# Optimization experiments

Measured on AMD Instinct MI355X. Metric: run time of the kernel, lower is better.

## Reference

```python
import jax, jax.numpy as jnp
import numpy as np

D = 1024
H = 16
HD = D // H
FF = 4 * D


def layer_norm(x, gamma, beta, eps=1e-5):
    mu = jnp.mean(x, axis=-1, keepdims=True)
    var = jnp.var(x, axis=-1, keepdims=True)
    return (x - mu) * jax.lax.rsqrt(var + eps) * gamma + beta


def setup_inputs() -> dict:
    key = jax.random.key(0)
    ks = jax.random.split(key, 12)
    B, Nq, Nkv = 8, 512, 1024
    s = 0.02
    return {
        "query": jax.random.normal(ks[0], (B, Nq, D), jnp.float32),
        "key_value": jax.random.normal(ks[1], (B, Nkv, D), jnp.float32),
        "key_padding_mask": jax.random.randint(ks[2], (B, Nkv), 0, 2) > 0,
        "nq_gamma": jnp.ones((D,), jnp.float32),
        "nq_beta": jnp.zeros((D,), jnp.float32),
        "nkv_gamma": jnp.ones((D,), jnp.float32),
        "nkv_beta": jnp.zeros((D,), jnp.float32),
        "in_proj_w": jax.random.normal(ks[3], (3 * D, D), jnp.float32) * s,
        "in_proj_b": jnp.zeros((3 * D,), jnp.float32),
        "out_w": jax.random.normal(ks[4], (D, D), jnp.float32) * s,
        "out_b": jnp.zeros((D,), jnp.float32),
        "nff_gamma": jnp.ones((D,), jnp.float32),
        "nff_beta": jnp.zeros((D,), jnp.float32),
        "ff1_w": jax.random.normal(ks[5], (FF, D), jnp.float32) * s,
        "ff1_b": jnp.zeros((FF,), jnp.float32),
        "ff2_w": jax.random.normal(ks[6], (D, FF), jnp.float32) * s,
        "ff2_b": jnp.zeros((D,), jnp.float32),
    }


def reference(query, key_value, key_padding_mask, nq_gamma, nq_beta, nkv_gamma,
              nkv_beta, in_proj_w, in_proj_b, out_w, out_b, nff_gamma, nff_beta,
              ff1_w, ff1_b, ff2_w, ff2_b):
    B, Nq, _ = query.shape
    Nkv = key_value.shape[1]

    q_in = layer_norm(query, nq_gamma, nq_beta)
    kv_in = layer_norm(key_value, nkv_gamma, nkv_beta)

    # packed in-projection as in torch MultiheadAttention
    wq, wk, wv = in_proj_w[:D], in_proj_w[D:2 * D], in_proj_w[2 * D:]
    bq, bk, bv = in_proj_b[:D], in_proj_b[D:2 * D], in_proj_b[2 * D:]
    q = (q_in @ wq.T + bq).reshape(B, Nq, H, HD).transpose(0, 2, 1, 3)   # b h q d
    k = (kv_in @ wk.T + bk).reshape(B, Nkv, H, HD).transpose(0, 2, 1, 3)  # b h k d
    v = (kv_in @ wv.T + bv).reshape(B, Nkv, H, HD).transpose(0, 2, 1, 3)

    scale = 1.0 / np.sqrt(HD).astype(np.float32)
    scores = jnp.einsum('bhqd,bhkd->bhqk', q, k) * scale
    neg = jnp.finfo(scores.dtype).min
    scores = jnp.where(key_padding_mask[:, None, None, :], neg, scores)
    attn = jax.nn.softmax(scores, axis=-1)                  # (B,H,Nq,Nkv)
    ctx = jnp.einsum('bhqk,bhkd->bhqd', attn, v)
    ctx = ctx.transpose(0, 2, 1, 3).reshape(B, Nq, D)
    attended = ctx @ out_w.T + out_b
    attn_weights = jnp.mean(attn, axis=1)                   # averaged over heads

    x = query + attended
    h = layer_norm(x, nff_gamma, nff_beta)
    h = jax.nn.gelu(h @ ff1_w.T + ff1_b, approximate=False)
    x = x + (h @ ff2_w.T + ff2_b)
    return (x, attn_weights)
```

## Files before the change

### kernel.cpp

```cpp
#include <hip/hip_runtime.h>
#include <hip/hip_bf16.h>
#include <math.h>

#define D    1024
#define NQ   512
#define NKV  1024
#define BATCH 8
#define NH   16
#define HD   64
#define FFD  4096

typedef short bf16x8 __attribute__((ext_vector_type(8)));
typedef float f32x4  __attribute__((ext_vector_type(4)));

static __device__ __forceinline__ float bf2f(__hip_bfloat16 x){ return __bfloat162float(x); }
static __device__ __forceinline__ unsigned short f2bbits(float f){
    __hip_bfloat16 h = __float2bfloat16(f);
    return *(unsigned short*)&h;
}

static __device__ __forceinline__ void gload_lds16(const __hip_bfloat16* g, __hip_bfloat16* l){
    __builtin_amdgcn_global_load_lds(
        (const __attribute__((address_space(1))) void*)g,
        (__attribute__((address_space(3))) void*)l,
        16, 0, 0);
}

__global__ __launch_bounds__(256) void cvt_w_kernel(const float* __restrict__ in,
                                                    __hip_bfloat16* __restrict__ out, int n)
{
    int i = blockIdx.x*256 + threadIdx.x;
    if (i < n) out[i] = __float2bfloat16(in[i]);
}

__global__ __launch_bounds__(256) void ln_kernel(
    const float* __restrict__ x, const float* __restrict__ gamma, const float* __restrict__ beta,
    __hip_bfloat16* __restrict__ out)
{
    int row = blockIdx.x, t = threadIdx.x;
    __shared__ float wsum[4];
    __shared__ float stat[2];
    float4 v = *(const float4*)&x[(size_t)row*D + t*4];
    float s = v.x+v.y+v.z+v.w;
    #pragma unroll
    for (int o=32;o>0;o>>=1) s += __shfl_down(s, o);
    if ((t&63)==0) wsum[t>>6] = s;
    __syncthreads();
    if (t==0) stat[0] = (wsum[0]+wsum[1]+wsum[2]+wsum[3])*(1.f/D);
    __syncthreads();
    float mu = stat[0];
    float d0=v.x-mu, d1=v.y-mu, d2=v.z-mu, d3=v.w-mu;
    float s2 = d0*d0+d1*d1+d2*d2+d3*d3;
    #pragma unroll
    for (int o=32;o>0;o>>=1) s2 += __shfl_down(s2, o);
    if ((t&63)==0) wsum[t>>6] = s2;
    __syncthreads();
    if (t==0) stat[1] = rsqrtf((wsum[0]+wsum[1]+wsum[2]+wsum[3])*(1.f/D) + 1e-5f);
    __syncthreads();
    float rs = stat[1];
    const float4 g = *(const float4*)&gamma[t*4];
    const float4 b = *(const float4*)&beta[t*4];
    union { unsigned short u[4]; short4 s4; } pk;
    pk.u[0]=f2bbits(d0*rs*g.x+b.x); pk.u[1]=f2bbits(d1*rs*g.y+b.y);
    pk.u[2]=f2bbits(d2*rs*g.z+b.z); pk.u[3]=f2bbits(d3*rs*g.w+b.w);
    *(short4*)&out[(size_t)row*D + t*4] = pk.s4;
}

#define BM 128
#define BN 128
#define BK 32
__global__ __launch_bounds__(256) void gemm_mfma_kernel(
    const __hip_bfloat16* __restrict__ A, const __hip_bfloat16* __restrict__ Wb,
    const float* __restrict__ bias, int biasOff,
    const float* __restrict__ residIn, const float* __restrict__ residF,
    float* __restrict__ Cf, __hip_bfloat16* __restrict__ Cb,
    int M, int N, int K, int gelu, int vtrans)
{
    __shared__ __hip_bfloat16 As[BM*BK];
    __shared__ __hip_bfloat16 Bs[BN*BK];
    int t = threadIdx.x;
    int w = t >> 6, lane = t & 63;
    int quad = lane >> 4, l16 = lane & 15;
    int bm = blockIdx.y * BM, bn = blockIdx.x * BN;
    int wm = (w >> 1) * 64, wn = (w & 1) * 64;
    const int srow = lane >> 2, scol = (lane & 3) << 3;
    f32x4 acc[4][4];
    #pragma unroll
    for (int i=0;i<4;i++)
        #pragma unroll
        for (int j=0;j<4;j++) acc[i][j] = (f32x4){0.f,0.f,0.f,0.f};

    for (int k0 = 0; k0 < K; k0 += BK){
        #pragma unroll
        for (int rep = 0; rep < 2; rep++){
            int ti = (w << 1) + rep;
            gload_lds16(&A [(size_t)(bm + ti*16 + srow)*K + k0 + scol], &As[ti*16*BK]);
            gload_lds16(&Wb[(size_t)(bn + ti*16 + srow)*K + k0 + scol], &Bs[ti*16*BK]);
        }
        __syncthreads();
        bf16x8 af[4], bfr[4];
        #pragma unroll
        for (int i=0;i<4;i++) af[i]  = *(const bf16x8*)&As[(wm + 16*i + l16)*BK + quad*8];
        #pragma unroll
        for (int j=0;j<4;j++) bfr[j] = *(const bf16x8*)&Bs[(wn + 16*j + l16)*BK + quad*8];
        #pragma unroll
        for (int i=0;i<4;i++)
            #pragma unroll
            for (int j=0;j<4;j++)
                acc[i][j] = __builtin_amdgcn_mfma_f32_16x16x32_bf16(af[i], bfr[j], acc[i][j], 0, 0, 0);
        __syncthreads();
    }
    #pragma unroll
    for (int i=0;i<4;i++){
        #pragma unroll
        for (int j=0;j<4;j++){
            int colg = bn + wn + 16*j + l16;
            if (vtrans){
                union { unsigned short u[4]; short4 s4; } pk;
                #pragma unroll
                for (int r=0;r<4;r++){
                    float vv = acc[i][j][r] + bias[biasOff + colg];
                    pk.u[r] = f2bbits(vv);
                }
                int rowg0 = bm + wm + 16*i + quad*4;
                int bb = rowg0 >> 10, kv = rowg0 & 1023;
                int hh = colg >> 6,  dd = colg & 63;
                *(short4*)&Cb[(((size_t)bb*NH + hh)*HD + dd)*NKV + kv] = pk.s4;
            } else {
                #pragma unroll
                for (int r=0;r<4;r++){
                    int rowg = bm + wm + 16*i + quad*4 + r;
                    float vv = acc[i][j][r] + bias[biasOff + colg];
                    if (gelu) vv = 0.5f*vv*(1.f + erff(vv*0.70710678118654752f));
                    size_t idx = (size_t)rowg*N + colg;
                    if (residIn) vv += residIn[idx];
                    if (residF)  vv += residF[idx];
                    if (Cf) Cf[idx] = vv;
                    if (Cb) Cb[idx] = __float2bfloat16(vv);
                }
            }
        }
    }
}

#define QT 16
#define PLD (NKV + 8)
__global__ __launch_bounds__(512) void attn_kernel(
    const __hip_bfloat16* __restrict__ q, const __hip_bfloat16* __restrict__ k,
    const __hip_bfloat16* __restrict__ vt, const void* __restrict__ mask,
    __hip_bfloat16* __restrict__ ctx, float* __restrict__ attn_out)
{
    const int t = threadIdx.x;
    const int w = t >> 6;
    const int lane = t & 63;
    const int g = lane >> 4;
    const int l16 = lane & 15;
    const int b  = blockIdx.x;
    const int q0 = blockIdx.y * QT;

    __shared__ __hip_bfloat16 P[QT*PLD];
    __shared__ float pvred[4*16*20];
    __shared__ float red[8*16];
    __shared__ int m8s;

    if (t==0) m8s = 0;
    __syncthreads();
    if (t < 256){ unsigned wd = ((const unsigned*)mask)[t]; if (wd > 1u) atomicOr(&m8s, 1); }
    __syncthreads();
    const bool m8 = m8s != 0;

    unsigned mbits = 0;
    #pragma unroll
    for (int kt=0;kt<8;kt++){
        #pragma unroll
        for (int r=0;r<4;r++){
            size_t mi = (size_t)b*NKV + w*128 + kt*16 + 4*g + r;
            int mv = m8 ? (int)((const unsigned char*)mask)[mi] : ((const int*)mask)[mi];
            if (mv) mbits |= (1u << (kt*4+r));
        }
    }

    float amean[8][4];
    #pragma unroll
    for (int kt=0;kt<8;kt++)
        #pragma unroll
        for (int r=0;r<4;r++) amean[kt][r] = 0.f;

    const int mt = w >> 1;
    const int kvh = w & 1;
    const __hip_bfloat16* qrow = &q[((size_t)(b*NQ + q0 + l16))*D];

    for (int h=0; h<NH; h++){
        bf16x8 bq0 = *(const bf16x8*)&qrow[h*HD + g*8];
        bf16x8 bq1 = *(const bf16x8*)&qrow[h*HD + 32 + g*8];
        f32x4 s[8];
        #pragma unroll
        for (int kt=0;kt<8;kt++){
            const __hip_bfloat16* kp = &k[((size_t)(b*NKV + w*128 + kt*16 + l16))*D + h*HD];
            bf16x8 a0 = *(const bf16x8*)&kp[g*8];
            bf16x8 a1 = *(const bf16x8*)&kp[32 + g*8];
            f32x4 z = (f32x4){0.f,0.f,0.f,0.f};
            z = __builtin_amdgcn_mfma_f32_16x16x32_bf16(a0, bq0, z, 0, 0, 0);
            z = __builtin_amdgcn_mfma_f32_16x16x32_bf16(a1, bq1, z, 0, 0, 0);
            s[kt] = z;
        }
        float lmax = -3.0e38f;
        #pragma unroll
        for (int kt=0;kt<8;kt++){
            #pragma unroll
            for (int r=0;r<4;r++){
                float sv = ((mbits >> (kt*4+r)) & 1u) ? -3.0e38f : s[kt][r]*0.125f;
                s[kt][r] = sv;
                lmax = fmaxf(lmax, sv);
            }
        }
        lmax = fmaxf(lmax, __shfl_xor(lmax, 16));
        lmax = fmaxf(lmax, __shfl_xor(lmax, 32));
        if (lane < 16) red[w*16 + l16] = lmax;
        __syncthreads();
        float m = red[l16];
        #pragma unroll
        for (int w2=1; w2<8; w2++) m = fmaxf(m, red[w2*16 + l16]);
        float lsum = 0.f;
        #pragma unroll
        for (int kt=0;kt<8;kt++){
            #pragma unroll
            for (int r=0;r<4;r++){
                float e = __expf(s[kt][r] - m);
                s[kt][r] = e;
                lsum += e;
            }
        }
        lsum += __shfl_xor(lsum, 16);
        lsum += __shfl_xor(lsum, 32);
        __syncthreads();
        if (lane < 16) red[w*16 + l16] = lsum;
        __syncthreads();
        float tot = red[l16];
        #pragma unroll
        for (int w2=1; w2<8; w2++) tot += red[w2*16 + l16];
        float inv = 1.f/tot;
        float ai  = inv * (1.f/NH);
        #pragma unroll
        for (int kt=0;kt<8;kt++){
            union { unsigned short u[4]; short4 s4; } pk;
            #pragma unroll
            for (int r=0;r<4;r++){
                amean[kt][r] += s[kt][r]*ai;
                pk.u[r] = f2bbits(s[kt][r]);
            }
            *(short4*)&P[l16*PLD + w*128 + kt*16 + 4*g] = pk.s4;
        }
        __syncthreads();
        f32x4 pv = (f32x4){0.f,0.f,0.f,0.f};
        const __hip_bfloat16* vrow = &vt[(((size_t)(b*NH + h))*HD + mt*16 + l16)*NKV + kvh*512];
        #pragma unroll
        for (int ks=0;ks<16;ks++){
            bf16x8 av = *(const bf16x8*)&vrow[ks*32 + g*8];
            bf16x8 bp = *(const bf16x8*)&P[l16*PLD + kvh*512 + ks*32 + g*8];
            pv = __builtin_amdgcn_mfma_f32_16x16x32_bf16(av, bp, pv, 0, 0, 0);
        }
        if (kvh){
            *(f32x4*)&pvred[(mt*16 + l16)*20 + 4*g] = pv;
        }
        __syncthreads();
        if (!kvh){
            const f32x4 other = *(const f32x4*)&pvred[(mt*16 + l16)*20 + 4*g];
            union { unsigned short u[4]; short4 s4; } pk;
            #pragma unroll
            for (int r=0;r<4;r++) pk.u[r] = f2bbits((pv[r] + other[r]) * inv);
            *(short4*)&ctx[((size_t)(b*NQ + q0 + l16))*D + h*HD + mt*16 + 4*g] = pk.s4;
        }
        __syncthreads();
    }
    float* ao = attn_out + ((size_t)(b*NQ + q0 + l16))*NKV;
    #pragma unroll
    for (int kt=0;kt<8;kt++){
        float4 v4 = make_float4(amean[kt][0], amean[kt][1], amean[kt][2], amean[kt][3]);
        *(float4*)&ao[w*128 + kt*16 + 4*g] = v4;
    }
}

__global__ __launch_bounds__(256) void fill_f32_kernel(float* __restrict__ p, float val, long n){
    size_t i = (size_t)blockIdx.x*256 + threadIdx.x;
    if ((long)i < n) p[i] = val;
}

extern "C" void kernel_launch(void* const* d_in, const int* in_sizes, int n_in,
                              void* d_out, int out_size, void* d_ws, size_t ws_size,
                              hipStream_t stream)
{
    const float* query     = (const float*)d_in[0];
    const float* key_value = (const float*)d_in[1];
    const void*  mask      = d_in[2];
    const float* nq_gamma  = (const float*)d_in[3];
    const float* nq_beta   = (const float*)d_in[4];
    const float* nkv_gamma = (const float*)d_in[5];
    const float* nkv_beta  = (const float*)d_in[6];
    const float* ipw       = (const float*)d_in[7];
    const float* ipb       = (const float*)d_in[8];
    const float* out_w     = (const float*)d_in[9];
    const float* out_b     = (const float*)d_in[10];
    const float* nffg      = (const float*)d_in[11];
    const float* nffb      = (const float*)d_in[12];
    const float* ff1w      = (const float*)d_in[13];
    const float* ff1b      = (const float*)d_in[14];
    const float* ff2w      = (const float*)d_in[15];
    const float* ff2b      = (const float*)d_in[16];

    float* out_x = (float*)d_out;
    long Dn  = (n_in > 3)  ? in_sizes[3]  : 0;
    long FFn = (n_in > 14) ? in_sizes[14] : 0;
    long Rq=0, Rkv=0, Nkvd=0, Bd=0, Nqd=0;
    auto derive = [&](long Sq_, long Skv_)->bool{
        if (Dn <= 0 || Sq_ <= 0 || Skv_ <= 0) return false;
        if (Sq_ % Dn || Skv_ % Dn) return false;
        Rq = Sq_/Dn; Rkv = Skv_/Dn;
        long num = (long)out_size - Rq*Dn;
        if (Rq <= 0 || num <= 0 || num % Rq) return false;
        Nkvd = num / Rq;
        if (Nkvd <= 0 || Rkv % Nkvd) return false;
        Bd = Rkv / Nkvd;
        if (Bd <= 0 || Rq % Bd) return false;
        Nqd = Rq / Bd;
        if ((long)in_sizes[2] != Rkv) return false;
        return true;
    };
    int sentinel = 0;
    if (n_in != 17) sentinel = 600;
    else if (!derive(in_sizes[0], in_sizes[1])) sentinel = 300;
    if (!sentinel && !(Dn==1024 && FFn==4096 && Bd==8 && Nqd==512 && Nkvd==1024)) sentinel = 500;
    if (!sentinel && ws_size < ((size_t)88<<20)) sentinel = 400;
    if (sentinel){
        long n = out_size;
        fill_f32_kernel<<<(unsigned)((n+255)/256), 256, 0, stream>>>(out_x, (float)sentinel, n);
        return;
    }

    float* out_attn = out_x + (size_t)BATCH*NQ*D;

    char* Wc = (char*)d_ws;
    __hip_bfloat16* wip  = (__hip_bfloat16*)(Wc);
    __hip_bfloat16* wout = (__hip_bfloat16*)(Wc + ((size_t)6<<20));
    __hip_bfloat16* wff1 = (__hip_bfloat16*)(Wc + ((size_t)8<<20));
    __hip_bfloat16* wff2 = (__hip_bfloat16*)(Wc + ((size_t)16<<20));
    __hip_bfloat16* qln  = (__hip_bfloat16*)(Wc + ((size_t)24<<20));
    __hip_bfloat16* kvln = (__hip_bfloat16*)(Wc + ((size_t)32<<20));
    __hip_bfloat16* qb   = (__hip_bfloat16*)(Wc + ((size_t)48<<20));
    __hip_bfloat16* kb   = (__hip_bfloat16*)(Wc + ((size_t)56<<20));
    __hip_bfloat16* vbT  = (__hip_bfloat16*)(Wc + ((size_t)72<<20));
    __hip_bfloat16* ctx  = (__hip_bfloat16*)(Wc + ((size_t)24<<20));
    float*          x1   = (float*)(Wc + ((size_t)32<<20));
    __hip_bfloat16* hln  = (__hip_bfloat16*)(Wc + ((size_t)48<<20));
    __hip_bfloat16* hge  = (__hip_bfloat16*)(Wc + ((size_t)56<<20));

    cvt_w_kernel<<<(3*1024*1024+255)/256, 256, 0, stream>>>(ipw,  wip,  3*1024*1024);
    cvt_w_kernel<<<(1024*1024+255)/256,   256, 0, stream>>>(out_w, wout, 1024*1024);
    cvt_w_kernel<<<(4*1024*1024+255)/256, 256, 0, stream>>>(ff1w, wff1, 4*1024*1024);
    cvt_w_kernel<<<(4*1024*1024+255)/256, 256, 0, stream>>>(ff2w, wff2, 4*1024*1024);
    ln_kernel<<<BATCH*NQ,  256, 0, stream>>>(query,     nq_gamma,  nq_beta,  qln);
    ln_kernel<<<BATCH*NKV, 256, 0, stream>>>(key_value, nkv_gamma, nkv_beta, kvln);
    gemm_mfma_kernel<<<dim3(8,32),  256, 0, stream>>>(qln,  wip,                 ipb, 0,   nullptr, nullptr, nullptr, qb,  4096, 1024, 1024, 0, 0);
    gemm_mfma_kernel<<<dim3(8,64),  256, 0, stream>>>(kvln, wip + (size_t)D*D,   ipb, D,   nullptr, nullptr, nullptr, kb,  8192, 1024, 1024, 0, 0);
    gemm_mfma_kernel<<<dim3(8,64),  256, 0, stream>>>(kvln, wip + (size_t)2*D*D, ipb, 2*D, nullptr, nullptr, nullptr, vbT, 8192, 1024, 1024, 0, 1);
    attn_kernel<<<dim3(BATCH, NQ/QT), 512, 0, stream>>>(qb, kb, vbT, mask, ctx, out_attn);
    gemm_mfma_kernel<<<dim3(8,32),  256, 0, stream>>>(ctx, wout, out_b, 0, query, nullptr, x1, nullptr, 4096, 1024, 1024, 0, 0);
    ln_kernel<<<4096, 256, 0, stream>>>(x1, nffg, nffb, hln);
    gemm_mfma_kernel<<<dim3(32,32), 256, 0, stream>>>(hln, wff1, ff1b, 0, nullptr, nullptr, nullptr, hge, 4096, 4096, 1024, 1, 0);
    gemm_mfma_kernel<<<dim3(8,32),  256, 0, stream>>>(hge, wff2, ff2b, 0, nullptr, x1, out_x, nullptr, 4096, 1024, 4096, 0, 0);
}
```

Before: 690.9 us.

## Double-buffer GEMM LDS staging and merge Q/K/V projections into one launch

The GEMM main loop now uses two LDS buffers, so the async global-to-LDS load of the next K tile is issued before the MFMA work on the current tile, overlapping memory with compute and halving barriers per tile. The three separate Q, K and V projection launches are replaced by one qkv_kernel with a flat grid. In that grid the K and V projections share one GEMM over the packed weight rows (N=2048), and the epilogue routes columns to K or to transposed V. The change doubles LDS use per block, which may reduce occupancy, and adds some register pressure from the extra staging.

```diff
diff --git a/kernel.cpp b/kernel.cpp
--- a/kernel.cpp
+++ b/kernel.cpp
@@ -69,75 +69,155 @@
 #define BM 128
 #define BN 128
 #define BK 32
+
+static __device__ __forceinline__ void stage128(
+    const __hip_bfloat16* __restrict__ A, const __hip_bfloat16* __restrict__ W,
+    int K, int bm, int bn, int k0,
+    __hip_bfloat16* as, __hip_bfloat16* bs, int w, int srow, int scol)
+{
+    #pragma unroll
+    for (int rep=0; rep<2; rep++){
+        int ti = (w<<1) + rep;
+        gload_lds16(&A[(size_t)(bm + ti*16 + srow)*K + k0 + scol], &as[ti*16*BK]);
+        gload_lds16(&W[(size_t)(bn + ti*16 + srow)*K + k0 + scol], &bs[ti*16*BK]);
+    }
+}
+
+static __device__ __forceinline__ void compute128(
+    const __hip_bfloat16* as, const __hip_bfloat16* bs,
+    int wm, int wn, int quad, int l16, f32x4 acc[4][4])
+{
+    bf16x8 af[4], bfr[4];
+    #pragma unroll
+    for (int i=0;i<4;i++) af[i]  = *(const bf16x8*)&as[(wm + 16*i + l16)*BK + quad*8];
+    #pragma unroll
+    for (int j=0;j<4;j++) bfr[j] = *(const bf16x8*)&bs[(wn + 16*j + l16)*BK + quad*8];
+    #pragma unroll
+    for (int i=0;i<4;i++)
+        #pragma unroll
+        for (int j=0;j<4;j++)
+            acc[i][j] = __builtin_amdgcn_mfma_f32_16x16x32_bf16(af[i], bfr[j], acc[i][j], 0, 0, 0);
+}
+
+static __device__ __forceinline__ void gemm_loop(
+    const __hip_bfloat16* __restrict__ A, const __hip_bfloat16* __restrict__ W,
+    int K, int bm, int bn,
+    __hip_bfloat16* As0, __hip_bfloat16* Bs0, __hip_bfloat16* As1, __hip_bfloat16* Bs1,
+    f32x4 acc[4][4])
+{
+    const int t = threadIdx.x;
+    const int w = t >> 6, lane = t & 63;
+    const int quad = lane >> 4, l16 = lane & 15;
+    const int wm = (w >> 1) * 64, wn = (w & 1) * 64;
+    const int srow = lane >> 2, scol = (lane & 3) << 3;
+
+    stage128(A, W, K, bm, bn, 0, As0, Bs0, w, srow, scol);
+    __syncthreads();
+    const int nt = K >> 5;
+    for (int ts = 0; ts < nt; ts += 2){
+        stage128(A, W, K, bm, bn, (ts+1)<<5, As1, Bs1, w, srow, scol);
+        compute128(As0, Bs0, wm, wn, quad, l16, acc);
+        __syncthreads();
+        if (ts + 2 < nt)
+            stage128(A, W, K, bm, bn, (ts+2)<<5, As0, Bs0, w, srow, scol);
+        compute128(As1, Bs1, wm, wn, quad, l16, acc);
+        __syncthreads();
+    }
+}
+
 __global__ __launch_bounds__(256) void gemm_mfma_kernel(
     const __hip_bfloat16* __restrict__ A, const __hip_bfloat16* __restrict__ Wb,
     const float* __restrict__ bias, int biasOff,
     const float* __restrict__ residIn, const float* __restrict__ residF,
     float* __restrict__ Cf, __hip_bfloat16* __restrict__ Cb,
-    int M, int N, int K, int gelu, int vtrans)
-{
-    __shared__ __hip_bfloat16 As[BM*BK];
-    __shared__ __hip_bfloat16 Bs[BN*BK];
-    int t = threadIdx.x;
-    int w = t >> 6, lane = t & 63;
-    int quad = lane >> 4, l16 = lane & 15;
+    int M, int N, int K, int gelu)
+{
+    __shared__ __hip_bfloat16 As0[BM*BK], Bs0[BN*BK], As1[BM*BK], Bs1[BN*BK];
     int bm = blockIdx.y * BM, bn = blockIdx.x * BN;
-    int wm = (w >> 1) * 64, wn = (w & 1) * 64;
-    const int srow = lane >> 2, scol = (lane & 3) << 3;
     f32x4 acc[4][4];
     #pragma unroll
     for (int i=0;i<4;i++)
         #pragma unroll
         for (int j=0;j<4;j++) acc[i][j] = (f32x4){0.f,0.f,0.f,0.f};
 
-    for (int k0 = 0; k0 < K; k0 += BK){
-        #pragma unroll
-        for (int rep = 0; rep < 2; rep++){
-            int ti = (w << 1) + rep;
-            gload_lds16(&A [(size_t)(bm + ti*16 + srow)*K + k0 + scol], &As[ti*16*BK]);
-            gload_lds16(&Wb[(size_t)(bn + ti*16 + srow)*K + k0 + scol], &Bs[ti*16*BK]);
-        }
-        __syncthreads();
-        bf16x8 af[4], bfr[4];
-        #pragma unroll
-        for (int i=0;i<4;i++) af[i]  = *(const bf16x8*)&As[(wm + 16*i + l16)*BK + quad*8];
-        #pragma unroll
-        for (int j=0;j<4;j++) bfr[j] = *(const bf16x8*)&Bs[(wn + 16*j + l16)*BK + quad*8];
-        #pragma unroll
-        for (int i=0;i<4;i++)
-            #pragma unroll
-            for (int j=0;j<4;j++)
-                acc[i][j] = __builtin_amdgcn_mfma_f32_16x16x32_bf16(af[i], bfr[j], acc[i][j], 0, 0, 0);
-        __syncthreads();
-    }
+    gemm_loop(A, Wb, K, bm, bn, As0, Bs0, As1, Bs1, acc);
+
+    const int t = threadIdx.x;
+    const int w = t >> 6, lane = t & 63;
+    const int quad = lane >> 4, l16 = lane & 15;
+    const int wm = (w >> 1) * 64, wn = (w & 1) * 64;
     #pragma unroll
     for (int i=0;i<4;i++){
         #pragma unroll
         for (int j=0;j<4;j++){
             int colg = bn + wn + 16*j + l16;
-            if (vtrans){
-                union { unsigned short u[4]; short4 s4; } pk;
-                #pragma unroll
-                for (int r=0;r<4;r++){
-                    float vv = acc[i][j][r] + bias[biasOff + colg];
-                    pk.u[r] = f2bbits(vv);
-                }
-                int rowg0 = bm + wm + 16*i + quad*4;
-                int bb = rowg0 >> 10, kv = rowg0 & 1023;
-                int hh = colg >> 6,  dd = colg & 63;
-                *(short4*)&Cb[(((size_t)bb*NH + hh)*HD + dd)*NKV + kv] = pk.s4;
-            } else {
+            float bv = bias[biasOff + colg];
+            #pragma unroll
+            for (int r=0;r<4;r++){
+                int rowg = bm + wm + 16*i + quad*4 + r;
+                float vv = acc[i][j][r] + bv;
+                if (gelu) vv = 0.5f*vv*(1.f + erff(vv*0.70710678118654752f));
+                size_t idx = (size_t)rowg*N + colg;
+                if (residIn) vv += residIn[idx];
+                if (residF)  vv += residF[idx];
+                if (Cf) Cf[idx] = vv;
+                if (Cb) Cb[idx] = __float2bfloat16(vv);
+            }
+        }
+    }
+}
+
+__global__ __launch_bounds__(256) void qkv_kernel(
+    const __hip_bfloat16* __restrict__ qln, const __hip_bfloat16* __restrict__ kvln,
+    const __hip_bfloat16* __restrict__ wip, const float* __restrict__ ipb,
+    __hip_bfloat16* __restrict__ qb, __hip_bfloat16* __restrict__ kb,
+    __hip_bfloat16* __restrict__ vbT)
+{
+    __shared__ __hip_bfloat16 As0[BM*BK], Bs0[BN*BK], As1[BM*BK], Bs1[BN*BK];
+    int id = blockIdx.x;
+    const __hip_bfloat16 *A, *W;
+    int bm, bn, isq;
+    if (id < 1024){ isq = 0; A = kvln; W = wip + (size_t)D*D; bn = (id & 15)*BN; bm = (id >> 4)*BM; }
+    else { int qid = id - 1024; isq = 1; A = qln; W = wip; bn = (qid & 7)*BN; bm = (qid >> 3)*BM; }
+
+    f32x4 acc[4][4];
+    #pragma unroll
+    for (int i=0;i<4;i++)
+        #pragma unroll
+        for (int j=0;j<4;j++) acc[i][j] = (f32x4){0.f,0.f,0.f,0.f};
+
+    gemm_loop(A, W, 1024, bm, bn, As0, Bs0, As1, Bs1, acc);
+
+    const int t = threadIdx.x;
+    const int w = t >> 6, lane = t & 63;
+    const int quad = lane >> 4, l16 = lane & 15;
+    const int wm = (w >> 1) * 64, wn = (w & 1) * 64;
+    #pragma unroll
+    for (int i=0;i<4;i++){
+        #pragma unroll
+        for (int j=0;j<4;j++){
+            int colg = bn + wn + 16*j + l16;
+            float bv = ipb[(isq ? 0 : D) + colg];
+            if (isq){
                 #pragma unroll
                 for (int r=0;r<4;r++){
                     int rowg = bm + wm + 16*i + quad*4 + r;
-                    float vv = acc[i][j][r] + bias[biasOff + colg];
-                    if (gelu) vv = 0.5f*vv*(1.f + erff(vv*0.70710678118654752f));
-                    size_t idx = (size_t)rowg*N + colg;
-                    if (residIn) vv += residIn[idx];
-                    if (residF)  vv += residF[idx];
-                    if (Cf) Cf[idx] = vv;
-                    if (Cb) Cb[idx] = __float2bfloat16(vv);
+                    qb[(size_t)rowg*D + colg] = __float2bfloat16(acc[i][j][r] + bv);
                 }
+            } else if (colg < 1024){
+                #pragma unroll
+                for (int r=0;r<4;r++){
+                    int rowg = bm + wm + 16*i + quad*4 + r;
+                    kb[(size_t)rowg*D + colg] = __float2bfloat16(acc[i][j][r] + bv);
+                }
+            } else {
+                union { unsigned short u[4]; short4 s4; } pk;
+                #pragma unroll
+                for (int r=0;r<4;r++) pk.u[r] = f2bbits(acc[i][j][r] + bv);
+                int rowg0 = bm + wm + 16*i + quad*4;
+                int bb = rowg0 >> 10, kvi = rowg0 & 1023;
+                int c = colg - 1024, hh = c >> 6, dd = c & 63;
+                *(short4*)&vbT[(((size_t)bb*NH + hh)*HD + dd)*NKV + kvi] = pk.s4;
             }
         }
     }
@@ -360,12 +440,10 @@
     cvt_w_kernel<<<(4*1024*1024+255)/256, 256, 0, stream>>>(ff2w, wff2, 4*1024*1024);
     ln_kernel<<<BATCH*NQ,  256, 0, stream>>>(query,     nq_gamma,  nq_beta,  qln);
     ln_kernel<<<BATCH*NKV, 256, 0, stream>>>(key_value, nkv_gamma, nkv_beta, kvln);
-    gemm_mfma_kernel<<<dim3(8,32),  256, 0, stream>>>(qln,  wip,                 ipb, 0,   nullptr, nullptr, nullptr, qb,  4096, 1024, 1024, 0, 0);
-    gemm_mfma_kernel<<<dim3(8,64),  256, 0, stream>>>(kvln, wip + (size_t)D*D,   ipb, D,   nullptr, nullptr, nullptr, kb,  8192, 1024, 1024, 0, 0);
-    gemm_mfma_kernel<<<dim3(8,64),  256, 0, stream>>>(kvln, wip + (size_t)2*D*D, ipb, 2*D, nullptr, nullptr, nullptr, vbT, 8192, 1024, 1024, 0, 1);
+    qkv_kernel<<<1280, 256, 0, stream>>>(qln, kvln, wip, ipb, qb, kb, vbT);
     attn_kernel<<<dim3(BATCH, NQ/QT), 512, 0, stream>>>(qb, kb, vbT, mask, ctx, out_attn);
-    gemm_mfma_kernel<<<dim3(8,32),  256, 0, stream>>>(ctx, wout, out_b, 0, query, nullptr, x1, nullptr, 4096, 1024, 1024, 0, 0);
+    gemm_mfma_kernel<<<dim3(8,32),  256, 0, stream>>>(ctx, wout, out_b, 0, query, nullptr, x1, nullptr, 4096, 1024, 1024, 0);
     ln_kernel<<<4096, 256, 0, stream>>>(x1, nffg, nffb, hln);
-    gemm_mfma_kernel<<<dim3(32,32), 256, 0, stream>>>(hln, wff1, ff1b, 0, nullptr, nullptr, nullptr, hge, 4096, 4096, 1024, 1, 0);
-    gemm_mfma_kernel<<<dim3(8,32),  256, 0, stream>>>(hge, wff2, ff2b, 0, nullptr, x1, out_x, nullptr, 4096, 1024, 4096, 0, 0);
-}
+    gemm_mfma_kernel<<<dim3(32,32), 256, 0, stream>>>(hln, wff1, ff1b, 0, nullptr, nullptr, nullptr, hge, 4096, 4096, 1024, 1);
+    gemm_mfma_kernel<<<dim3(8,32),  256, 0, stream>>>(hge, wff2, ff2b, 0, nullptr, x1, out_x, nullptr, 4096, 1024, 4096, 0);
+}
```

After: 607.9 us. -12.0%, faster.
